# Performance work log

Hardware: AMD Instinct MI355X
Metric: run time of the kernel (lower is better)

## Reference

```python
import jax, jax.numpy as jnp
import numpy as np

B, S, D, H = 2, 2048, 1024, 16
DK = D // H  # 64
SCALE = DK ** (-0.5)  # NOTE: module divides by this, i.e. multiplies scores by sqrt(DK)


def setup_inputs() -> dict:
    key = jax.random.key(0)
    ks = jax.random.split(key, 9)
    std = D ** (-0.5)
    return {
        "x": jax.random.normal(ks[0], (B, S, D), dtype=jnp.float32),
        "attention_mask": jnp.ones((B, S), dtype=jnp.int32),
        "Wq": jax.random.normal(ks[1], (D, D), dtype=jnp.float32) * std,
        "bq": jnp.zeros((D,), dtype=jnp.float32),
        "Wk": jax.random.normal(ks[2], (D, D), dtype=jnp.float32) * std,
        "bk": jnp.zeros((D,), dtype=jnp.float32),
        "Wv": jax.random.normal(ks[3], (D, D), dtype=jnp.float32) * std,
        "bv": jnp.zeros((D,), dtype=jnp.float32),
        "Wo": jax.random.normal(ks[4], (D, D), dtype=jnp.float32) * std,
        "bo": jnp.zeros((D,), dtype=jnp.float32),
    }


def _split_heads(t):
    # [B, S, D] -> [B, H, S, DK]
    return t.reshape(B, S, H, DK).transpose(0, 2, 1, 3)


def reference(x, attention_mask, Wq, bq, Wk, bk, Wv, bv, Wo, bo):
    q = _split_heads(x @ Wq.T + bq)
    k = _split_heads(x @ Wk.T + bk)
    v = _split_heads(x @ Wv.T + bv)

    # faithful to source: sim = (q @ k^T) / scale with scale = dk**-0.5
    sim = jnp.einsum("bhqd,bhkd->bhqk", q, k) / SCALE

    # key-padding mask: positions where attention_mask == 0 are masked out
    neg = jnp.finfo(sim.dtype).min
    keep = attention_mask.astype(bool)[:, None, None, :]  # [B,1,1,S]
    sim = jnp.where(keep, sim, neg)

    attn = jax.nn.softmax(sim, axis=-1)  # dropout is identity at inference
    out = jnp.einsum("bhqk,bhkd->bhqd", attn, v)
    out = out.transpose(0, 2, 1, 3).reshape(B, S, D)  # merge heads
    return out @ Wo.T + bo
```

## Files before the change

### kernel.cpp

```cpp
#include <hip/hip_runtime.h>
#include <hip/hip_bf16.h>
#include <math.h>

#define BB 2
#define SS 2048
#define DD 1024
#define HH 16
#define DKK 64
#define BH (BB * HH)

typedef __bf16 bf16_t;
typedef _Float16 f16_t;
typedef __attribute__((ext_vector_type(8))) _Float16 f16x8;
typedef __attribute__((ext_vector_type(4))) _Float16 f16x4;
typedef __attribute__((ext_vector_type(4))) float f32x4;
typedef __attribute__((ext_vector_type(4))) int i32x4;
typedef __attribute__((ext_vector_type(2))) int i32x2;

#define GLD_LDS(gp, lp) __builtin_amdgcn_global_load_lds( \
    (const __attribute__((address_space(1))) void*)(gp),  \
    (__attribute__((address_space(3))) void*)(lp), 16, 0, 0)

static __device__ __forceinline__ int pkrtz(float a, float b) {
    auto h = __builtin_amdgcn_cvt_pkrtz(a, b);
    return __builtin_bit_cast(int, h);
}

__global__ void cast_x_flags(const float* __restrict__ in, f16_t* __restrict__ out,
                             const int* __restrict__ mask, int* __restrict__ flags, int n) {
    int i = blockIdx.x * blockDim.x + threadIdx.x;
    int stride = gridDim.x * blockDim.x;
    for (; i < n; i += stride) out[i] = (f16_t)in[i];
    if (blockIdx.x == 0 && threadIdx.x < BB * (SS / 128)) {
        int f = threadIdx.x;
        int b = f / (SS / 128), t = f % (SS / 128);
        const int* p = mask + b * SS + t * 128;
        int all = 1;
        for (int j = 0; j < 128; ++j) all &= (p[j] != 0);
        flags[f] = all;
    }
}

__global__ void cast_wqk(const float* __restrict__ Wq, const float* __restrict__ Wk,
                         f16_t* __restrict__ hi, f16_t* __restrict__ lo, int nw) {
    int i = blockIdx.x * blockDim.x + threadIdx.x;
    int stride = gridDim.x * blockDim.x;
    for (; i < 2 * nw; i += stride) {
        float v = (i < nw) ? Wq[i] : Wk[i - nw];
        f16_t h = (f16_t)v;
        hi[i] = h;
        lo[i] = (f16_t)(v - (float)h);
    }
}

__global__ void cast_wvo(const float* __restrict__ Wv, const float* __restrict__ Wo,
                         f16_t* __restrict__ wv, f16_t* __restrict__ wo, int nw) {
    int i = blockIdx.x * blockDim.x + threadIdx.x;
    int stride = gridDim.x * blockDim.x;
    for (; i < 2 * nw; i += stride) {
        if (i < nw) wv[i] = (f16_t)Wv[i];
        else        wo[i - nw] = (f16_t)Wo[i - nw];
    }
}

__global__ __launch_bounds__(256) void gemm_qkv(const f16_t* __restrict__ Af,
                                                const f16_t* __restrict__ Wqkh,
                                                const f16_t* __restrict__ Wqkl,
                                                const f16_t* __restrict__ Wvf,
                                                const float* __restrict__ bq,
                                                const float* __restrict__ bk,
                                                const float* __restrict__ bv,
                                                f16_t* __restrict__ q_o,
                                                f16_t* __restrict__ k_o,
                                                f16_t* __restrict__ vt_o,
                                                int K) {
    __shared__ __align__(16) f16_t sA[4096];
    __shared__ __align__(16) f16_t sB0[4096];
    __shared__ __align__(16) f16_t sB1[4096];

    const int tid  = threadIdx.x;
    const int wv   = tid >> 6;
    const int lane = tid & 63;
    const int quad = lane >> 4;
    const int l15  = lane & 15;
    const int wr   = wv >> 1;
    const int wc   = wv & 1;
    const int row0 = blockIdx.y * 128;
    const int col0 = blockIdx.x * 128;
    const bool isV = (col0 >= 2048);

    const f16_t* B0 = isV ? (Wvf + (long)(col0 - 2048) * K) : (Wqkh + (long)col0 * K);
    const f16_t* B1 = isV ? nullptr : (Wqkl + (long)col0 * K);

    f32x4 acc[4][4] = {};

    const int srow = tid >> 2;
    const int scol = (tid & 3) * 8;
    const long aoff = (long)(row0 + srow) * K + scol;
    const long boff = (long)srow * K + scol;

    if (isV) {
#pragma unroll 1
        for (int kb = 0; kb < K; kb += 32) {
#pragma unroll
            for (int p = 0; p < 2; ++p) {
                const long go = (long)p * 64 * K + kb;
                const int lo = p * 2048 + wv * 512;
                GLD_LDS(Af + aoff + go, sA + lo);
                GLD_LDS(B0 + boff + go, sB0 + lo);
            }
            __syncthreads();
            f16x8 af[4];
#pragma unroll
            for (int mt = 0; mt < 4; ++mt)
                af[mt] = *(const f16x8*)&sA[(wr * 64 + mt * 16 + l15) * 32 + quad * 8];
#pragma unroll
            for (int nt = 0; nt < 4; ++nt) {
                f16x8 b0 = *(const f16x8*)&sB0[(wc * 64 + nt * 16 + l15) * 32 + quad * 8];
#pragma unroll
                for (int mt = 0; mt < 4; ++mt)
                    acc[mt][nt] = __builtin_amdgcn_mfma_f32_16x16x32_f16(af[mt], b0, acc[mt][nt], 0, 0, 0);
            }
            __syncthreads();
        }
    } else {
#pragma unroll 1
        for (int kb = 0; kb < K; kb += 32) {
#pragma unroll
            for (int p = 0; p < 2; ++p) {
                const long go = (long)p * 64 * K + kb;
                const int lo = p * 2048 + wv * 512;
                GLD_LDS(Af + aoff + go, sA + lo);
                GLD_LDS(B0 + boff + go, sB0 + lo);
                GLD_LDS(B1 + boff + go, sB1 + lo);
            }
            __syncthreads();
            f16x8 af[4];
#pragma unroll
            for (int mt = 0; mt < 4; ++mt)
                af[mt] = *(const f16x8*)&sA[(wr * 64 + mt * 16 + l15) * 32 + quad * 8];
#pragma unroll
            for (int nt = 0; nt < 4; ++nt) {
                f16x8 b0 = *(const f16x8*)&sB0[(wc * 64 + nt * 16 + l15) * 32 + quad * 8];
                f16x8 b1 = *(const f16x8*)&sB1[(wc * 64 + nt * 16 + l15) * 32 + quad * 8];
#pragma unroll
                for (int mt = 0; mt < 4; ++mt) {
                    acc[mt][nt] = __builtin_amdgcn_mfma_f32_16x16x32_f16(af[mt], b0, acc[mt][nt], 0, 0, 0);
                    acc[mt][nt] = __builtin_amdgcn_mfma_f32_16x16x32_f16(af[mt], b1, acc[mt][nt], 0, 0, 0);
                }
            }
            __syncthreads();
        }
    }

    if (isV) {
#pragma unroll
        for (int nt = 0; nt < 4; ++nt) {
            const int colv = (col0 - 2048) + wc * 64 + nt * 16 + l15;
            const float bvv = bv[colv];
            const int hq = colv >> 6, dk = colv & 63;
#pragma unroll
            for (int mt = 0; mt < 4; ++mt) {
                const int grow0 = row0 + wr * 64 + mt * 16 + quad * 4;
                const int bq2 = grow0 >> 11;
                const int s0  = grow0 & (SS - 1);
                f16x4 pk;
#pragma unroll
                for (int r = 0; r < 4; ++r) pk[r] = (f16_t)(acc[mt][nt][r] + bvv);
                *(f16x4*)(vt_o + ((long)(bq2 * HH + hq) * DKK + dk) * SS + s0) = pk;
            }
        }
    } else {
        const bool isK = (col0 >= 1024);
        const float* bias = isK ? bk : bq;
        f16_t* op = isK ? k_o : q_o;
#pragma unroll
        for (int nt = 0; nt < 4; ++nt) {
            const int gcol = (col0 & 1023) + wc * 64 + nt * 16 + l15;
            const float bvv = bias[gcol];
            const int hq = gcol >> 6, dk = gcol & 63;
#pragma unroll
            for (int mt = 0; mt < 4; ++mt) {
                const int grow0 = row0 + wr * 64 + mt * 16 + quad * 4;
#pragma unroll
                for (int r = 0; r < 4; ++r) {
                    int grow = grow0 + r;
                    float vvv = acc[mt][nt][r] + bvv;
                    long off = (((long)(grow >> 11) * HH + hq) * SS + (grow & (SS - 1))) * DKK + dk;
                    op[off] = (f16_t)vvv;
                }
            }
        }
    }
}

__global__ __launch_bounds__(256) void gemm_o(const f16_t* __restrict__ Ah,
                                              const f16_t* __restrict__ Bhp,
                                              const float* __restrict__ bias,
                                              float* __restrict__ outf,
                                              int N, int K) {
    __shared__ __align__(16) f16_t lds[2048 + 4096];
    f16_t* Ash = lds;
    f16_t* Bsh = lds + 2048;

    const int tid  = threadIdx.x;
    const int wv   = tid >> 6;
    const int lane = tid & 63;
    const int quad = lane >> 4;
    const int l15  = lane & 15;
    const int wr   = wv >> 1;
    const int wc   = wv & 1;
    const int row0 = blockIdx.y * 64;
    const int col0 = blockIdx.x * 128;

    f32x4 acc[2][4] = {};

    const int srow = lane >> 2;
    const int scol = (lane & 3) * 8;
    const f16_t* gA  = Ah  + (long)(row0 + wv * 16 + srow) * K + scol;
    const f16_t* gB0 = Bhp + (long)(col0 + wv * 16 + srow) * K + scol;
    const f16_t* gB1 = Bhp + (long)(col0 + (wv + 4) * 16 + srow) * K + scol;
    f16_t* lA  = Ash + wv * 512;
    f16_t* lB0 = Bsh + wv * 512;
    f16_t* lB1 = Bsh + (wv + 4) * 512;

#pragma unroll 1
    for (int kb = 0; kb < K; kb += 32) {
        GLD_LDS(gA + kb, lA);
        GLD_LDS(gB0 + kb, lB0);
        GLD_LDS(gB1 + kb, lB1);
        __syncthreads();

        f16x8 af[2];
#pragma unroll
        for (int mt = 0; mt < 2; ++mt)
            af[mt] = *(const f16x8*)&Ash[(wr * 32 + mt * 16 + l15) * 32 + quad * 8];
#pragma unroll
        for (int nt = 0; nt < 4; ++nt) {
            f16x8 bh = *(const f16x8*)&Bsh[(wc * 64 + nt * 16 + l15) * 32 + quad * 8];
#pragma unroll
            for (int mt = 0; mt < 2; ++mt)
                acc[mt][nt] = __builtin_amdgcn_mfma_f32_16x16x32_f16(af[mt], bh, acc[mt][nt], 0, 0, 0);
        }
        __syncthreads();
    }

#pragma unroll
    for (int mt = 0; mt < 2; ++mt) {
#pragma unroll
        for (int nt = 0; nt < 4; ++nt) {
            const int gcol  = col0 + wc * 64 + nt * 16 + l15;
            const float bvv = bias[gcol];
            const int grow0 = row0 + wr * 32 + mt * 16 + quad * 4;
#pragma unroll
            for (int r = 0; r < 4; ++r)
                outf[(long)(grow0 + r) * N + gcol] = acc[mt][nt][r] + bvv;
        }
    }
}

__global__ __launch_bounds__(256) void attn_mfma9(const f16_t* __restrict__ Qp,
                                                  const f16_t* __restrict__ Kp,
                                                  const f16_t* __restrict__ Vtp,
                                                  const int* __restrict__ mask,
                                                  const int* __restrict__ flags,
                                                  f16_t* __restrict__ ctx,
                                                  int seq_len) {
    __shared__ __align__(16) f16_t Ksh[2][2][4096];
    __shared__ __align__(16) f16_t Vsh[2][2][4096];

    const int tid  = threadIdx.x;
    const int wv   = tid >> 6;
    const int lane = tid & 63;
    const int quad = lane >> 4;
    const int l15  = lane & 15;
    const int bh   = blockIdx.y;
    const int b    = bh >> 4;
    const int h    = bh & 15;
    const int q0   = blockIdx.x * 128 + wv * 16;

    const long kb = (long)bh * SS * DKK;

    f16x8 qf0[2], qf1[2];
    {
        const f16_t* pq = Qp + kb + (long)(q0 + l15) * DKK + quad * 8;
        qf0[0] = *(const f16x8*)pq;
        qf0[1] = *(const f16x8*)(pq + 32);
        const f16_t* pq1 = pq + 64 * DKK;
        qf1[0] = *(const f16x8*)pq1;
        qf1[1] = *(const f16x8*)(pq1 + 32);
        const f16_t qs = (f16_t)(8.0f * 1.44269504088896f);
#pragma unroll
        for (int j = 0; j < 8; ++j) {
            qf0[0][j] *= qs; qf0[1][j] *= qs;
            qf1[0][j] *= qs; qf1[1][j] *= qs;
        }
    }

    f16x4 ones4;
#pragma unroll
    for (int j = 0; j < 4; ++j) ones4[j] = (f16_t)1.0f;

    f32x4 o0[4], o1[4], lacc0, lacc1;
#pragma unroll
    for (int r = 0; r < 4; ++r) {
        o0[r] = (f32x4){0.f, 0.f, 0.f, 0.f};
        o1[r] = (f32x4){0.f, 0.f, 0.f, 0.f};
    }
    lacc0 = (f32x4){0.f, 0.f, 0.f, 0.f};
    lacc1 = (f32x4){0.f, 0.f, 0.f, 0.f};
    float m0 = -1e30f, m1 = -1e30f;

    const int* mrow = mask + b * SS;
    const int* frow = flags + b * (SS / 128);

    const int srow8 = lane >> 3;
    const int gcolB = ((lane & 7) ^ srow8) * 8;
    const int NT = seq_len >> 7;

#pragma unroll
    for (int c = 0; c < 2; ++c) {
#pragma unroll
        for (int p = 0; p < 2; ++p) {
            const int i = wv * 2 + p;
            const int row = i * 8 + srow8;
            GLD_LDS(Kp + kb + (long)(c * 64 + row) * DKK + gcolB, &Ksh[0][c][i * 512]);
            GLD_LDS(Vtp + kb + (long)row * SS + c * 64 + gcolB, &Vsh[0][c][i * 512]);
        }
    }

#pragma unroll 1
    for (int tt = 0; tt < NT; ++tt) {
        const int cur = tt & 1;
        const int kt = tt << 7;
        __syncthreads();

        if (tt + 1 < NT) {
            const int kn = (tt + 1) << 7;
#pragma unroll
            for (int c = 0; c < 2; ++c) {
#pragma unroll
                for (int p = 0; p < 2; ++p) {
                    const int i = wv * 2 + p;
                    const int row = i * 8 + srow8;
                    GLD_LDS(Kp + kb + (long)(kn + c * 64 + row) * DKK + gcolB, &Ksh[cur ^ 1][c][i * 512]);
                    GLD_LDS(Vtp + kb + (long)row * SS + kn + c * 64 + gcolB, &Vsh[cur ^ 1][c][i * 512]);
                }
            }
        }

        f32x4 s0[8], s1[8];
#pragma unroll
        for (int nt = 0; nt < 8; ++nt) {
            s0[nt] = (f32x4){0.f, 0.f, 0.f, 0.f};
            s1[nt] = (f32x4){0.f, 0.f, 0.f, 0.f};
        }
#pragma unroll
        for (int nt = 0; nt < 8; ++nt) {
            const int c = nt >> 2;
            const int kr = (nt & 3) * 16 + l15;
#pragma unroll
            for (int dt = 0; dt < 2; ++dt) {
                f16x8 kf = *(const f16x8*)&Ksh[cur][c][kr * 64 + (((dt * 4 + quad) ^ (l15 & 7)) << 3)];
                s0[nt] = __builtin_amdgcn_mfma_f32_16x16x32_f16(kf, qf0[dt], s0[nt], 0, 0, 0);
                s1[nt] = __builtin_amdgcn_mfma_f32_16x16x32_f16(kf, qf1[dt], s1[nt], 0, 0, 0);
            }
        }

        if (!frow[kt >> 7]) {
#pragma unroll
            for (int nt = 0; nt < 8; ++nt) {
                i32x4 kp = *(const i32x4*)&mrow[kt + nt * 16 + quad * 4];
#pragma unroll
                for (int r = 0; r < 4; ++r) {
                    s0[nt][r] = kp[r] ? s0[nt][r] : -1e30f;
                    s1[nt][r] = kp[r] ? s1[nt][r] : -1e30f;
                }
            }
        }

        f32x4 mxa, mxb;
#pragma unroll
        for (int r = 0; r < 4; ++r) {
            mxa[r] = fmaxf(fmaxf(fmaxf(s0[0][r], s0[1][r]), fmaxf(s0[2][r], s0[3][r])),
                           fmaxf(fmaxf(s0[4][r], s0[5][r]), fmaxf(s0[6][r], s0[7][r])));
            mxb[r] = fmaxf(fmaxf(fmaxf(s1[0][r], s1[1][r]), fmaxf(s1[2][r], s1[3][r])),
                           fmaxf(fmaxf(s1[4][r], s1[5][r]), fmaxf(s1[6][r], s1[7][r])));
        }
        float tm0 = fmaxf(fmaxf(mxa[0], mxa[1]), fmaxf(mxa[2], mxa[3]));
        float tm1 = fmaxf(fmaxf(mxb[0], mxb[1]), fmaxf(mxb[2], mxb[3]));
        tm0 = fmaxf(tm0, __shfl_xor(tm0, 16));
        tm1 = fmaxf(tm1, __shfl_xor(tm1, 16));
        tm0 = fmaxf(tm0, __shfl_xor(tm0, 32));
        tm1 = fmaxf(tm1, __shfl_xor(tm1, 32));

        const float mn0 = fmaxf(m0, tm0);
        const float mn1 = fmaxf(m1, tm1);
        if (__any(tm0 > m0)) {
            const float alpha = exp2f(m0 - mn0);
            float a4[4];
#pragma unroll
            for (int r = 0; r < 4; ++r) a4[r] = __shfl(alpha, quad * 4 + r);
#pragma unroll
            for (int t = 0; t < 4; ++t)
#pragma unroll
                for (int r = 0; r < 4; ++r) o0[t][r] *= a4[r];
#pragma unroll
            for (int r = 0; r < 4; ++r) lacc0[r] *= a4[r];
        }
        if (__any(tm1 > m1)) {
            const float alpha = exp2f(m1 - mn1);
            float a4[4];
#pragma unroll
            for (int r = 0; r < 4; ++r) a4[r] = __shfl(alpha, quad * 4 + r);
#pragma unroll
            for (int t = 0; t < 4; ++t)
#pragma unroll
                for (int r = 0; r < 4; ++r) o1[t][r] *= a4[r];
#pragma unroll
            for (int r = 0; r < 4; ++r) lacc1[r] *= a4[r];
        }
        m0 = mn0;
        m1 = mn1;

#pragma unroll
        for (int nt = 0; nt < 8; ++nt) {
            const int c = nt >> 2;
            i32x2 pp0, pp1;
            pp0[0] = pkrtz(exp2f(s0[nt][0] - mn0), exp2f(s0[nt][1] - mn0));
            pp0[1] = pkrtz(exp2f(s0[nt][2] - mn0), exp2f(s0[nt][3] - mn0));
            pp1[0] = pkrtz(exp2f(s1[nt][0] - mn1), exp2f(s1[nt][1] - mn1));
            pp1[1] = pkrtz(exp2f(s1[nt][2] - mn1), exp2f(s1[nt][3] - mn1));
            f16x4 paf0 = __builtin_bit_cast(f16x4, pp0);
            f16x4 paf1 = __builtin_bit_cast(f16x4, pp1);
            lacc0 = __builtin_amdgcn_mfma_f32_16x16x16f16(paf0, ones4, lacc0, 0, 0, 0);
            lacc1 = __builtin_amdgcn_mfma_f32_16x16x16f16(paf1, ones4, lacc1, 0, 0, 0);
            const int vcol = ((((nt & 3) * 2 + (quad >> 1)) ^ (l15 & 7)) << 3) + ((quad & 1) << 2);
#pragma unroll
            for (int t = 0; t < 4; ++t) {
                f16x4 vB = *(const f16x4*)&Vsh[cur][c][(t * 16 + l15) * 64 + vcol];
                o0[t] = __builtin_amdgcn_mfma_f32_16x16x16f16(paf0, vB, o0[t], 0, 0, 0);
                o1[t] = __builtin_amdgcn_mfma_f32_16x16x16f16(paf1, vB, o1[t], 0, 0, 0);
            }
        }
    }

    float inv0[4], inv1[4];
#pragma unroll
    for (int r = 0; r < 4; ++r) {
        inv0[r] = 1.0f / lacc0[r];
        inv1[r] = 1.0f / lacc1[r];
    }
#pragma unroll
    for (int t = 0; t < 4; ++t) {
        int d = t * 16 + l15;
#pragma unroll
        for (int r = 0; r < 4; ++r) {
            int tok = b * SS + q0 + quad * 4 + r;
            ctx[(long)tok * DD + h * DKK + d] = (f16_t)(o0[t][r] * inv0[r]);
            ctx[(long)(tok + 64) * DD + h * DKK + d] = (f16_t)(o1[t][r] * inv1[r]);
        }
    }
}

extern "C" void kernel_launch(void* const* d_in, const int* in_sizes, int n_in,
                              void* d_out, int out_size, void* d_ws, size_t ws_size,
                              hipStream_t stream) {
    const float* x  = (const float*)d_in[0];
    const int* mask = (const int*)d_in[1];
    const float* Wq = (const float*)d_in[2];
    const float* bq = (const float*)d_in[3];
    const float* Wk = (const float*)d_in[4];
    const float* bk = (const float*)d_in[5];
    const float* Wv = (const float*)d_in[6];
    const float* bv = (const float*)d_in[7];
    const float* Wo = (const float*)d_in[8];
    const float* bo = (const float*)d_in[9];
    float* out = (float*)d_out;

    const long NX = (long)BB * SS * DD;
    const long NW = (long)DD * DD;

    char* ws = (char*)d_ws;
    f16_t* xf   = (f16_t*)ws; ws += NX * 2;
    f16_t* wqkh = (f16_t*)ws; ws += 2 * NW * 2;
    f16_t* wqkl = (f16_t*)ws; ws += 2 * NW * 2;
    f16_t* wvf  = (f16_t*)ws; ws += NW * 2;
    f16_t* wof  = (f16_t*)ws; ws += NW * 2;
    f16_t* qf   = (f16_t*)ws; ws += NX * 2;
    f16_t* kf   = (f16_t*)ws; ws += NX * 2;
    f16_t* vt   = (f16_t*)ws; ws += NX * 2;
    f16_t* ctx  = (f16_t*)ws; ws += NX * 2;
    int*   flg  = (int*)ws;   ws += 64 * 4;

    cast_x_flags<<<2048, 256, 0, stream>>>(x, xf, mask, flg, (int)NX);
    cast_wqk<<<2048, 256, 0, stream>>>(Wq, Wk, wqkh, wqkl, (int)NW);
    cast_wvo<<<2048, 256, 0, stream>>>(Wv, Wo, wvf, wof, (int)NW);

    dim3 gqkv(3 * DD / 128, (BB * SS) / 128);
    gemm_qkv<<<gqkv, 256, 0, stream>>>(xf, wqkh, wqkl, wvf, bq, bk, bv, qf, kf, vt, DD);

    dim3 agrid(SS / 128, BH);
    attn_mfma9<<<agrid, 256, 0, stream>>>(qf, kf, vt, mask, flg, ctx, SS);

    dim3 go(DD / 128, (BB * SS) / 64);
    gemm_o<<<go, 256, 0, stream>>>(ctx, wof, bo, out, DD, DD);
}
```

Baseline: 273.7 us.

## Single-buffer K tile in attention for occupancy and enlarge output GEMM tile

The attention kernel now keeps one K buffer instead of two. QK^T is computed first, then a barrier, then the next K/V tiles are prefetched, and launch bounds request three blocks per CU. This cuts LDS use so more blocks can be resident, at the cost of less overlap between the K load and compute. Separately, the output projection GEMM moves from 64x128 to 128x128 tiles, raising MFMA reuse per LDS load while halving the grid to 256 blocks.

```diff
diff --git a/kernel.cpp b/kernel.cpp
--- a/kernel.cpp
+++ b/kernel.cpp
@@ -199,9 +199,8 @@
                                               const float* __restrict__ bias,
                                               float* __restrict__ outf,
                                               int N, int K) {
-    __shared__ __align__(16) f16_t lds[2048 + 4096];
-    f16_t* Ash = lds;
-    f16_t* Bsh = lds + 2048;
+    __shared__ __align__(16) f16_t sA[4096];
+    __shared__ __align__(16) f16_t sB[4096];
 
     const int tid  = threadIdx.x;
     const int wv   = tid >> 6;
@@ -210,48 +209,47 @@
     const int l15  = lane & 15;
     const int wr   = wv >> 1;
     const int wc   = wv & 1;
-    const int row0 = blockIdx.y * 64;
+    const int row0 = blockIdx.y * 128;
     const int col0 = blockIdx.x * 128;
 
-    f32x4 acc[2][4] = {};
-
-    const int srow = lane >> 2;
-    const int scol = (lane & 3) * 8;
-    const f16_t* gA  = Ah  + (long)(row0 + wv * 16 + srow) * K + scol;
-    const f16_t* gB0 = Bhp + (long)(col0 + wv * 16 + srow) * K + scol;
-    const f16_t* gB1 = Bhp + (long)(col0 + (wv + 4) * 16 + srow) * K + scol;
-    f16_t* lA  = Ash + wv * 512;
-    f16_t* lB0 = Bsh + wv * 512;
-    f16_t* lB1 = Bsh + (wv + 4) * 512;
+    f32x4 acc[4][4] = {};
+
+    const int srow = tid >> 2;
+    const int scol = (tid & 3) * 8;
+    const long aoff = (long)(row0 + srow) * K + scol;
+    const long boff = (long)(col0 + srow) * K + scol;
 
 #pragma unroll 1
     for (int kb = 0; kb < K; kb += 32) {
-        GLD_LDS(gA + kb, lA);
-        GLD_LDS(gB0 + kb, lB0);
-        GLD_LDS(gB1 + kb, lB1);
+#pragma unroll
+        for (int p = 0; p < 2; ++p) {
+            const long go = (long)p * 64 * K + kb;
+            const int lo = p * 2048 + wv * 512;
+            GLD_LDS(Ah + aoff + go, sA + lo);
+            GLD_LDS(Bhp + boff + go, sB + lo);
+        }
         __syncthreads();
-
-        f16x8 af[2];
-#pragma unroll
-        for (int mt = 0; mt < 2; ++mt)
-            af[mt] = *(const f16x8*)&Ash[(wr * 32 + mt * 16 + l15) * 32 + quad * 8];
+        f16x8 af[4];
+#pragma unroll
+        for (int mt = 0; mt < 4; ++mt)
+            af[mt] = *(const f16x8*)&sA[(wr * 64 + mt * 16 + l15) * 32 + quad * 8];
 #pragma unroll
         for (int nt = 0; nt < 4; ++nt) {
-            f16x8 bh = *(const f16x8*)&Bsh[(wc * 64 + nt * 16 + l15) * 32 + quad * 8];
-#pragma unroll
-            for (int mt = 0; mt < 2; ++mt)
+            f16x8 bh = *(const f16x8*)&sB[(wc * 64 + nt * 16 + l15) * 32 + quad * 8];
+#pragma unroll
+            for (int mt = 0; mt < 4; ++mt)
                 acc[mt][nt] = __builtin_amdgcn_mfma_f32_16x16x32_f16(af[mt], bh, acc[mt][nt], 0, 0, 0);
         }
         __syncthreads();
     }
 
 #pragma unroll
-    for (int mt = 0; mt < 2; ++mt) {
-#pragma unroll
-        for (int nt = 0; nt < 4; ++nt) {
-            const int gcol  = col0 + wc * 64 + nt * 16 + l15;
-            const float bvv = bias[gcol];
-            const int grow0 = row0 + wr * 32 + mt * 16 + quad * 4;
+    for (int nt = 0; nt < 4; ++nt) {
+        const int gcol = col0 + wc * 64 + nt * 16 + l15;
+        const float bvv = bias[gcol];
+#pragma unroll
+        for (int mt = 0; mt < 4; ++mt) {
+            const int grow0 = row0 + wr * 64 + mt * 16 + quad * 4;
 #pragma unroll
             for (int r = 0; r < 4; ++r)
                 outf[(long)(grow0 + r) * N + gcol] = acc[mt][nt][r] + bvv;
@@ -259,14 +257,14 @@
     }
 }
 
-__global__ __launch_bounds__(256) void attn_mfma9(const f16_t* __restrict__ Qp,
-                                                  const f16_t* __restrict__ Kp,
-                                                  const f16_t* __restrict__ Vtp,
-                                                  const int* __restrict__ mask,
-                                                  const int* __restrict__ flags,
-                                                  f16_t* __restrict__ ctx,
-                                                  int seq_len) {
-    __shared__ __align__(16) f16_t Ksh[2][2][4096];
+__global__ __launch_bounds__(256, 3) void attn_mfma11(const f16_t* __restrict__ Qp,
+                                                      const f16_t* __restrict__ Kp,
+                                                      const f16_t* __restrict__ Vtp,
+                                                      const int* __restrict__ mask,
+                                                      const int* __restrict__ flags,
+                                                      f16_t* __restrict__ ctx,
+                                                      int seq_len) {
+    __shared__ __align__(16) f16_t Ksh[2][4096];
     __shared__ __align__(16) f16_t Vsh[2][2][4096];
 
     const int tid  = threadIdx.x;
@@ -324,7 +322,7 @@
         for (int p = 0; p < 2; ++p) {
             const int i = wv * 2 + p;
             const int row = i * 8 + srow8;
-            GLD_LDS(Kp + kb + (long)(c * 64 + row) * DKK + gcolB, &Ksh[0][c][i * 512]);
+            GLD_LDS(Kp + kb + (long)(c * 64 + row) * DKK + gcolB, &Ksh[c][i * 512]);
             GLD_LDS(Vtp + kb + (long)row * SS + c * 64 + gcolB, &Vsh[0][c][i * 512]);
         }
     }
@@ -335,6 +333,25 @@
         const int kt = tt << 7;
         __syncthreads();
 
+        f32x4 s0[8], s1[8];
+#pragma unroll
+        for (int nt = 0; nt < 8; ++nt) {
+            s0[nt] = (f32x4){0.f, 0.f, 0.f, 0.f};
+            s1[nt] = (f32x4){0.f, 0.f, 0.f, 0.f};
+        }
+#pragma unroll
+        for (int nt = 0; nt < 8; ++nt) {
+            const int c = nt >> 2;
+            const int kr = (nt & 3) * 16 + l15;
+#pragma unroll
+            for (int dt = 0; dt < 2; ++dt) {
+                f16x8 kf = *(const f16x8*)&Ksh[c][kr * 64 + (((dt * 4 + quad) ^ (l15 & 7)) << 3)];
+                s0[nt] = __builtin_amdgcn_mfma_f32_16x16x32_f16(kf, qf0[dt], s0[nt], 0, 0, 0);
+                s1[nt] = __builtin_amdgcn_mfma_f32_16x16x32_f16(kf, qf1[dt], s1[nt], 0, 0, 0);
+            }
+        }
+
+        __syncthreads();
         if (tt + 1 < NT) {
             const int kn = (tt + 1) << 7;
 #pragma unroll
@@ -343,27 +360,9 @@
                 for (int p = 0; p < 2; ++p) {
                     const int i = wv * 2 + p;
                     const int row = i * 8 + srow8;
-                    GLD_LDS(Kp + kb + (long)(kn + c * 64 + row) * DKK + gcolB, &Ksh[cur ^ 1][c][i * 512]);
+                    GLD_LDS(Kp + kb + (long)(kn + c * 64 + row) * DKK + gcolB, &Ksh[c][i * 512]);
                     GLD_LDS(Vtp + kb + (long)row * SS + kn + c * 64 + gcolB, &Vsh[cur ^ 1][c][i * 512]);
                 }
-            }
-        }
-
-        f32x4 s0[8], s1[8];
-#pragma unroll
-        for (int nt = 0; nt < 8; ++nt) {
-            s0[nt] = (f32x4){0.f, 0.f, 0.f, 0.f};
-            s1[nt] = (f32x4){0.f, 0.f, 0.f, 0.f};
-        }
-#pragma unroll
-        for (int nt = 0; nt < 8; ++nt) {
-            const int c = nt >> 2;
-            const int kr = (nt & 3) * 16 + l15;
-#pragma unroll
-            for (int dt = 0; dt < 2; ++dt) {
-                f16x8 kf = *(const f16x8*)&Ksh[cur][c][kr * 64 + (((dt * 4 + quad) ^ (l15 & 7)) << 3)];
-                s0[nt] = __builtin_amdgcn_mfma_f32_16x16x32_f16(kf, qf0[dt], s0[nt], 0, 0, 0);
-                s1[nt] = __builtin_amdgcn_mfma_f32_16x16x32_f16(kf, qf1[dt], s1[nt], 0, 0, 0);
             }
         }
 
@@ -501,8 +500,8 @@
     gemm_qkv<<<gqkv, 256, 0, stream>>>(xf, wqkh, wqkl, wvf, bq, bk, bv, qf, kf, vt, DD);
 
     dim3 agrid(SS / 128, BH);
-    attn_mfma9<<<agrid, 256, 0, stream>>>(qf, kf, vt, mask, flg, ctx, SS);
-
-    dim3 go(DD / 128, (BB * SS) / 64);
+    attn_mfma11<<<agrid, 256, 0, stream>>>(qf, kf, vt, mask, flg, ctx, SS);
+
+    dim3 go(DD / 128, (BB * SS) / 128);
     gemm_o<<<go, 256, 0, stream>>>(ctx, wof, bo, out, DD, DD);
 }
```

Measured after the change: 276.8 us. About the same (+1.1%).

## Single-buffer K tile in attention and fuse three cast kernels into one

Applied to the files above, without the earlier changes.

The attention kernel now keeps one K buffer instead of two. It computes QK^T from that buffer first, then synchronises and issues the prefetch of the next K tile, while V stays double-buffered. A launch-bounds hint of three blocks per CU is added. The smaller LDS footprint is meant to raise occupancy, but the K load for the next tile now overlaps only with softmax and PV rather than with the whole iteration, and there is an extra barrier. Separately, the three cast/prep kernels are merged into one launch to cut launch overhead.

```diff
diff --git a/kernel.cpp b/kernel.cpp
--- a/kernel.cpp
+++ b/kernel.cpp
@@ -26,40 +26,40 @@
     return __builtin_bit_cast(int, h);
 }
 
-__global__ void cast_x_flags(const float* __restrict__ in, f16_t* __restrict__ out,
-                             const int* __restrict__ mask, int* __restrict__ flags, int n) {
+__global__ void prep_all(const float* __restrict__ x, const int* __restrict__ mask,
+                         const float* __restrict__ Wq, const float* __restrict__ Wk,
+                         const float* __restrict__ Wv, const float* __restrict__ Wo,
+                         f16_t* __restrict__ xf,
+                         f16_t* __restrict__ wqkh, f16_t* __restrict__ wqkl,
+                         f16_t* __restrict__ wvf, f16_t* __restrict__ wof,
+                         int* __restrict__ flags) {
+    const int NXi = BB * SS * DD;
+    const int NWi = DD * DD;
+    const int total = NXi + 4 * NWi;
     int i = blockIdx.x * blockDim.x + threadIdx.x;
-    int stride = gridDim.x * blockDim.x;
-    for (; i < n; i += stride) out[i] = (f16_t)in[i];
+    const int stride = gridDim.x * blockDim.x;
+    for (; i < total; i += stride) {
+        if (i < NXi) {
+            xf[i] = (f16_t)x[i];
+        } else if (i < NXi + 2 * NWi) {
+            const int j = i - NXi;
+            const float v = (j < NWi) ? Wq[j] : Wk[j - NWi];
+            const f16_t h = (f16_t)v;
+            wqkh[j] = h;
+            wqkl[j] = (f16_t)(v - (float)h);
+        } else {
+            const int j = i - NXi - 2 * NWi;
+            if (j < NWi) wvf[j] = (f16_t)Wv[j];
+            else         wof[j - NWi] = (f16_t)Wo[j - NWi];
+        }
+    }
     if (blockIdx.x == 0 && threadIdx.x < BB * (SS / 128)) {
-        int f = threadIdx.x;
-        int b = f / (SS / 128), t = f % (SS / 128);
+        const int f = threadIdx.x;
+        const int b = f / (SS / 128), t = f % (SS / 128);
         const int* p = mask + b * SS + t * 128;
         int all = 1;
         for (int j = 0; j < 128; ++j) all &= (p[j] != 0);
         flags[f] = all;
-    }
-}
-
-__global__ void cast_wqk(const float* __restrict__ Wq, const float* __restrict__ Wk,
-                         f16_t* __restrict__ hi, f16_t* __restrict__ lo, int nw) {
-    int i = blockIdx.x * blockDim.x + threadIdx.x;
-    int stride = gridDim.x * blockDim.x;
-    for (; i < 2 * nw; i += stride) {
-        float v = (i < nw) ? Wq[i] : Wk[i - nw];
-        f16_t h = (f16_t)v;
-        hi[i] = h;
-        lo[i] = (f16_t)(v - (float)h);
-    }
-}
-
-__global__ void cast_wvo(const float* __restrict__ Wv, const float* __restrict__ Wo,
-                         f16_t* __restrict__ wv, f16_t* __restrict__ wo, int nw) {
-    int i = blockIdx.x * blockDim.x + threadIdx.x;
-    int stride = gridDim.x * blockDim.x;
-    for (; i < 2 * nw; i += stride) {
-        if (i < nw) wv[i] = (f16_t)Wv[i];
-        else        wo[i - nw] = (f16_t)Wo[i - nw];
     }
 }
 
@@ -259,14 +259,14 @@
     }
 }
 
-__global__ __launch_bounds__(256) void attn_mfma9(const f16_t* __restrict__ Qp,
-                                                  const f16_t* __restrict__ Kp,
-                                                  const f16_t* __restrict__ Vtp,
-                                                  const int* __restrict__ mask,
-                                                  const int* __restrict__ flags,
-                                                  f16_t* __restrict__ ctx,
-                                                  int seq_len) {
-    __shared__ __align__(16) f16_t Ksh[2][2][4096];
+__global__ __launch_bounds__(256, 3) void attn_mfma11(const f16_t* __restrict__ Qp,
+                                                      const f16_t* __restrict__ Kp,
+                                                      const f16_t* __restrict__ Vtp,
+                                                      const int* __restrict__ mask,
+                                                      const int* __restrict__ flags,
+                                                      f16_t* __restrict__ ctx,
+                                                      int seq_len) {
+    __shared__ __align__(16) f16_t Ksh[2][4096];
     __shared__ __align__(16) f16_t Vsh[2][2][4096];
 
     const int tid  = threadIdx.x;
@@ -324,7 +324,7 @@
         for (int p = 0; p < 2; ++p) {
             const int i = wv * 2 + p;
             const int row = i * 8 + srow8;
-            GLD_LDS(Kp + kb + (long)(c * 64 + row) * DKK + gcolB, &Ksh[0][c][i * 512]);
+            GLD_LDS(Kp + kb + (long)(c * 64 + row) * DKK + gcolB, &Ksh[c][i * 512]);
             GLD_LDS(Vtp + kb + (long)row * SS + c * 64 + gcolB, &Vsh[0][c][i * 512]);
         }
     }
@@ -335,6 +335,25 @@
         const int kt = tt << 7;
         __syncthreads();
 
+        f32x4 s0[8], s1[8];
+#pragma unroll
+        for (int nt = 0; nt < 8; ++nt) {
+            s0[nt] = (f32x4){0.f, 0.f, 0.f, 0.f};
+            s1[nt] = (f32x4){0.f, 0.f, 0.f, 0.f};
+        }
+#pragma unroll
+        for (int nt = 0; nt < 8; ++nt) {
+            const int c = nt >> 2;
+            const int kr = (nt & 3) * 16 + l15;
+#pragma unroll
+            for (int dt = 0; dt < 2; ++dt) {
+                f16x8 kf = *(const f16x8*)&Ksh[c][kr * 64 + (((dt * 4 + quad) ^ (l15 & 7)) << 3)];
+                s0[nt] = __builtin_amdgcn_mfma_f32_16x16x32_f16(kf, qf0[dt], s0[nt], 0, 0, 0);
+                s1[nt] = __builtin_amdgcn_mfma_f32_16x16x32_f16(kf, qf1[dt], s1[nt], 0, 0, 0);
+            }
+        }
+
+        __syncthreads();
         if (tt + 1 < NT) {
             const int kn = (tt + 1) << 7;
 #pragma unroll
@@ -343,27 +362,9 @@
                 for (int p = 0; p < 2; ++p) {
                     const int i = wv * 2 + p;
                     const int row = i * 8 + srow8;
-                    GLD_LDS(Kp + kb + (long)(kn + c * 64 + row) * DKK + gcolB, &Ksh[cur ^ 1][c][i * 512]);
+                    GLD_LDS(Kp + kb + (long)(kn + c * 64 + row) * DKK + gcolB, &Ksh[c][i * 512]);
                     GLD_LDS(Vtp + kb + (long)row * SS + kn + c * 64 + gcolB, &Vsh[cur ^ 1][c][i * 512]);
                 }
-            }
-        }
-
-        f32x4 s0[8], s1[8];
-#pragma unroll
-        for (int nt = 0; nt < 8; ++nt) {
-            s0[nt] = (f32x4){0.f, 0.f, 0.f, 0.f};
-            s1[nt] = (f32x4){0.f, 0.f, 0.f, 0.f};
-        }
-#pragma unroll
-        for (int nt = 0; nt < 8; ++nt) {
-            const int c = nt >> 2;
-            const int kr = (nt & 3) * 16 + l15;
-#pragma unroll
-            for (int dt = 0; dt < 2; ++dt) {
-                f16x8 kf = *(const f16x8*)&Ksh[cur][c][kr * 64 + (((dt * 4 + quad) ^ (l15 & 7)) << 3)];
-                s0[nt] = __builtin_amdgcn_mfma_f32_16x16x32_f16(kf, qf0[dt], s0[nt], 0, 0, 0);
-                s1[nt] = __builtin_amdgcn_mfma_f32_16x16x32_f16(kf, qf1[dt], s1[nt], 0, 0, 0);
             }
         }
 
@@ -493,15 +494,14 @@
     f16_t* ctx  = (f16_t*)ws; ws += NX * 2;
     int*   flg  = (int*)ws;   ws += 64 * 4;
 
-    cast_x_flags<<<2048, 256, 0, stream>>>(x, xf, mask, flg, (int)NX);
-    cast_wqk<<<2048, 256, 0, stream>>>(Wq, Wk, wqkh, wqkl, (int)NW);
-    cast_wvo<<<2048, 256, 0, stream>>>(Wv, Wo, wvf, wof, (int)NW);
+    prep_all<<<2048, 256, 0, stream>>>(x, mask, Wq, Wk, Wv, Wo,
+                                       xf, wqkh, wqkl, wvf, wof, flg);
 
     dim3 gqkv(3 * DD / 128, (BB * SS) / 128);
     gemm_qkv<<<gqkv, 256, 0, stream>>>(xf, wqkh, wqkl, wvf, bq, bk, bv, qf, kf, vt, DD);
 
     dim3 agrid(SS / 128, BH);
-    attn_mfma9<<<agrid, 256, 0, stream>>>(qf, kf, vt, mask, flg, ctx, SS);
+    attn_mfma11<<<agrid, 256, 0, stream>>>(qf, kf, vt, mask, flg, ctx, SS);
 
     dim3 go(DD / 128, (BB * SS) / 64);
     gemm_o<<<go, 256, 0, stream>>>(ctx, wof, bo, out, DD, DD);
```

Result: no change. 277.7 us (+1.4%).
